# Kernel optimization log

Measured on AMD Instinct MI355X. Metric: run time of the kernel, lower is better.

Reference implementation:

```python
import jax, jax.numpy as jnp
import numpy as np

D = 1024
H = 16
HD = D // H
LN_EPS = 1e-5
RMS_EPS = 1e-6


def layernorm(x, g, b):
    mu = jnp.mean(x, axis=-1, keepdims=True)
    var = jnp.mean(jnp.square(x - mu), axis=-1, keepdims=True)
    return (x - mu) * jax.lax.rsqrt(var + LN_EPS) * g + b


def rmsnorm(x, w):
    ms = jnp.mean(jnp.square(x), axis=-1, keepdims=True)
    return x * jax.lax.rsqrt(ms + RMS_EPS) * w


def setup_inputs() -> dict:
    key = jax.random.key(0)
    ks = jax.random.split(key, 8)
    s = 0.02
    ones = jnp.ones((D,), jnp.float32)
    zeros = jnp.zeros((D,), jnp.float32)
    return {
        "query_tokens": jax.random.normal(ks[0], (4, 512, D), jnp.float32),
        "point_features": jax.random.normal(ks[1], (4, 4096, D), jnp.float32),
        "ln_q_g": ones, "ln_q_b": zeros,
        "ln_kv_g": ones, "ln_kv_b": zeros,
        "Wq": jax.random.normal(ks[2], (D, D), jnp.float32) * s, "bq": zeros,
        "Wk": jax.random.normal(ks[3], (D, D), jnp.float32) * s, "bk": zeros,
        "Wv": jax.random.normal(ks[4], (D, D), jnp.float32) * s, "bv": zeros,
        "rms_q_w": ones, "rms_k_w": ones,
        "Wo": jax.random.normal(ks[5], (D, D), jnp.float32) * s, "bo": zeros,
        "ln_mlp_g": ones, "ln_mlp_b": zeros,
        "W1": jax.random.normal(ks[6], (D, 4 * D), jnp.float32) * s,
        "b1": jnp.zeros((4 * D,), jnp.float32),
        "W2": jax.random.normal(ks[7], (4 * D, D), jnp.float32) * s,
        "b2": zeros,
    }


def reference(query_tokens, point_features, ln_q_g, ln_q_b, ln_kv_g, ln_kv_b,
              Wq, bq, Wk, bk, Wv, bv, rms_q_w, rms_k_w, Wo, bo,
              ln_mlp_g, ln_mlp_b, W1, b1, W2, b2):
    B, K, _ = query_tokens.shape
    N = point_features.shape[1]
    q_in = layernorm(query_tokens, ln_q_g, ln_q_b)
    kv_in = layernorm(point_features, ln_kv_g, ln_kv_b)
    q = rmsnorm(q_in @ Wq + bq, rms_q_w)          # [B,K,D]
    k = rmsnorm(kv_in @ Wk + bk, rms_k_w)         # [B,N,D]
    v = kv_in @ Wv + bv                            # [B,N,D]
    q = q.reshape(B, K, H, HD)
    k = k.reshape(B, N, H, HD)
    v = v.reshape(B, N, H, HD)
    scores = jnp.einsum('bkhd,bnhd->bhkn', q, k) / jnp.sqrt(jnp.float32(HD))
    attn = jax.nn.softmax(scores, axis=-1)
    ctx = jnp.einsum('bhkn,bnhd->bkhd', attn, v).reshape(B, K, D)
    out = ctx @ Wo + bo + query_tokens
    h = layernorm(out, ln_mlp_g, ln_mlp_b)
    mlp = jax.nn.gelu(h @ W1 + b1, approximate=False) @ W2 + b2
    return out + mlp
```

## Files before the change

### kernel.cpp

```cpp
#include <hip/hip_runtime.h>
#include <math.h>

#define DD   1024
#define NHD  16
#define HDIM 64
#define BB   4
#define QN   512
#define KVN  4096
#define FF   4096

typedef __attribute__((ext_vector_type(8))) short bf16x8;
typedef __attribute__((ext_vector_type(4))) float f32x4;

__device__ __forceinline__ float b2f(ushort u){
  union { unsigned u32; float f; } x; x.u32 = ((unsigned)u)<<16; return x.f;
}
__device__ __forceinline__ ushort f2b(float f){
  unsigned u = __float_as_uint(f);
  unsigned r = (u + 0x7FFFu + ((u>>16)&1u)) >> 16;
  return (ushort)r;
}
__device__ __forceinline__ float ldx(const void* p, size_t i, int isbf){
  return isbf ? b2f(((const ushort*)p)[i]) : ((const float*)p)[i];
}
__device__ __forceinline__ int detect_bf(const void* gref){
  return ((const unsigned*)gref)[0] == 0x3F803F80u;
}

#if defined(__has_builtin)
#if __has_builtin(__builtin_amdgcn_global_load_lds)
#define HAS_GLL 1
#endif
#endif
#ifndef HAS_GLL
#define HAS_GLL 0
#endif
__device__ __forceinline__ void stage16(const ushort* g, ushort* lds_base, int lane){
#if HAS_GLL
  __builtin_amdgcn_global_load_lds(g, lds_base, 16, 0, 0);
#else
  *(uint4*)(lds_base + lane*8) = *(const uint4*)g;
#endif
}

__device__ __forceinline__ void wave_barrier(){
  asm volatile("" ::: "memory");
  __builtin_amdgcn_s_barrier();
  asm volatile("" ::: "memory");
}

__global__ __launch_bounds__(256)
void prep_all(const void* __restrict__ Wq, const void* __restrict__ Wk,
              const void* __restrict__ Wv, const void* __restrict__ Wo,
              const void* __restrict__ W1, const void* __restrict__ W2,
              ushort* __restrict__ WqT, ushort* __restrict__ WkvT,
              ushort* __restrict__ WoT,
              ushort* __restrict__ W1T, ushort* __restrict__ W2T,
              const void* __restrict__ qtok, const void* __restrict__ pfeat,
              const void* __restrict__ gq, const void* __restrict__ bq,
              const void* __restrict__ gkv, const void* __restrict__ bkv,
              ushort* __restrict__ q_ln, ushort* __restrict__ kv_ln,
              const void* __restrict__ gref)
{
  const int isbf = detect_bf(gref);
  __shared__ __align__(16) ushort tile[64][72];
  __shared__ float r1[4], r2[4];
  int t = threadIdx.x;

  if (blockIdx.x < 3072){
    int bid = blockIdx.x;
    const void* src; ushort* dst; int R, C, tid;
    if (bid < 1024){
      int s = bid >> 8; tid = bid & 255; R = 1024; C = 1024;
      src = (s==0) ? Wq : (s==1) ? Wk : (s==2) ? Wv : Wo;
      dst = (s==0) ? WqT : (s==1) ? WkvT : (s==2) ? (WkvT + (size_t)1024*1024) : WoT;
    } else if (bid < 2048){ tid = bid - 1024; src = W1; dst = W1T; R = 1024; C = 4096; }
    else                  { tid = bid - 2048; src = W2; dst = W2T; R = 4096; C = 1024; }
    int ntx = C >> 6;
    int tx = tid % ntx, ty = tid / ntx;
    int r0 = ty*64, c0 = tx*64;

    if (isbf){
      #pragma unroll
      for (int i=0;i<2;i++){
        int idx = t + i*256;
        int r = idx>>3, ch = idx&7;
        #pragma unroll
        for (int j=0;j<8;j++)
          tile[r][ch*8+j] = ((const ushort*)src)[(size_t)(r0+r)*C + c0 + ch*8 + j];
      }
    } else {
      #pragma unroll
      for (int i=0;i<2;i++){
        int idx = t + i*256;
        int r = idx>>3, ch = idx&7;
        const float* s4 = (const float*)src + (size_t)(r0+r)*C + c0 + ch*8;
        float4 f0 = *(const float4*)s4;
        float4 f1 = *(const float4*)(s4+4);
        tile[r][ch*8+0]=f2b(f0.x); tile[r][ch*8+1]=f2b(f0.y);
        tile[r][ch*8+2]=f2b(f0.z); tile[r][ch*8+3]=f2b(f0.w);
        tile[r][ch*8+4]=f2b(f1.x); tile[r][ch*8+5]=f2b(f1.y);
        tile[r][ch*8+6]=f2b(f1.z); tile[r][ch*8+7]=f2b(f1.w);
      }
    }
    __syncthreads();
    #pragma unroll
    for (int i=0;i<2;i++){
      int idx = t + i*256;
      int c = idx>>3, ch = idx&7;
      __align__(16) ushort tmp[8];
      #pragma unroll
      for (int j=0;j<8;j++) tmp[j] = tile[ch*8+j][c];
      *(uint4*)(dst + (size_t)(c0+c)*R + r0 + ch*8) = *(uint4*)tmp;
    }
    return;
  }

  int row = blockIdx.x - 3072;
  const void* src; const void* g; const void* bb; ushort* dst; int r;
  if (row < BB*QN){ src = qtok;  g = gq;  bb = bq;  dst = q_ln;  r = row; }
  else            { src = pfeat; g = gkv; bb = bkv; dst = kv_ln; r = row - BB*QN; }
  int c0 = t*4;
  float v[4];
  if (isbf){
    #pragma unroll
    for (int i=0;i<4;i++) v[i] = b2f(((const ushort*)src)[(size_t)r*DD + c0 + i]);
  } else {
    float4 f = *(const float4*)((const float*)src + (size_t)r*DD + c0);
    v[0]=f.x; v[1]=f.y; v[2]=f.z; v[3]=f.w;
  }
  float s1=0.f, s2=0.f;
  #pragma unroll
  for (int i=0;i<4;i++){ s1 += v[i]; s2 += v[i]*v[i]; }
  #pragma unroll
  for (int off=32; off; off>>=1){ s1 += __shfl_xor(s1,off,64); s2 += __shfl_xor(s2,off,64); }
  int wave = t>>6;
  if ((t&63)==0){ r1[wave]=s1; r2[wave]=s2; }
  __syncthreads();
  s1 = r1[0]+r1[1]+r1[2]+r1[3];
  s2 = r2[0]+r2[1]+r2[2]+r2[3];
  float mu  = s1 * (1.0f/DD);
  float var = s2 * (1.0f/DD) - mu*mu;
  float rs  = rsqrtf(var + 1e-5f);
  union { ushort u[4]; uint2 w; } pk;
  #pragma unroll
  for (int i=0;i<4;i++)
    pk.u[i] = f2b((v[i]-mu)*rs*ldx(g,c0+i,isbf) + ldx(bb,c0+i,isbf));
  *(uint2*)(dst + (size_t)r*DD + c0) = pk.w;
}

__global__ __launch_bounds__(256)
void rms_all(ushort* __restrict__ qb, const void* __restrict__ wq,
             ushort* __restrict__ kb, const void* __restrict__ wk,
             const void* __restrict__ gref)
{
  const int isbf = detect_bf(gref);
  int row = blockIdx.x, t = threadIdx.x;
  ushort* x; const void* w; int r;
  if (row < BB*QN){ x = qb; w = wq; r = row; }
  else            { x = kb; w = wk; r = row - BB*QN; }
  int c0 = t*4;
  union { ushort u[4]; uint2 w; } in;
  in.w = *(const uint2*)(x + (size_t)r*DD + c0);
  float v[4];
  #pragma unroll
  for (int i=0;i<4;i++) v[i] = b2f(in.u[i]);
  float s2 = 0.f;
  #pragma unroll
  for (int i=0;i<4;i++) s2 += v[i]*v[i];
  #pragma unroll
  for (int off=32; off; off>>=1) s2 += __shfl_xor(s2,off,64);
  __shared__ float r2[4];
  int wave = t>>6;
  if ((t&63)==0) r2[wave]=s2;
  __syncthreads();
  s2 = r2[0]+r2[1]+r2[2]+r2[3];
  float rs = rsqrtf(s2*(1.0f/DD) + 1e-6f);
  union { ushort u[4]; uint2 w; } pk;
  #pragma unroll
  for (int i=0;i<4;i++) pk.u[i] = f2b(v[i]*rs*ldx(w,c0+i,isbf));
  *(uint2*)(x + (size_t)r*DD + c0) = pk.w;
}

__global__ __launch_bounds__(256)
void ln_combine(const float* __restrict__ parts,
                const void* __restrict__ bo, const void* __restrict__ qtok,
                const void* __restrict__ g, const void* __restrict__ bb,
                float* __restrict__ outb, ushort* __restrict__ y,
                const void* __restrict__ gref)
{
  const int isbf = detect_bf(gref);
  const size_t PSZ = (size_t)BB*QN*DD;
  int row = blockIdx.x, t = threadIdx.x;
  int c0 = t*4;
  size_t base = (size_t)row*DD + c0;
  float v[4] = {0.f,0.f,0.f,0.f};
  #pragma unroll
  for (int z=0; z<4; z++){
    float4 p = *(const float4*)(parts + (size_t)z*PSZ + base);
    v[0]+=p.x; v[1]+=p.y; v[2]+=p.z; v[3]+=p.w;
  }
  if (isbf){
    #pragma unroll
    for (int i=0;i<4;i++)
      v[i] += b2f(((const ushort*)qtok)[base+i]) + b2f(((const ushort*)bo)[c0+i]);
  } else {
    float4 q4 = *(const float4*)((const float*)qtok + base);
    v[0] += q4.x + ((const float*)bo)[c0+0];
    v[1] += q4.y + ((const float*)bo)[c0+1];
    v[2] += q4.z + ((const float*)bo)[c0+2];
    v[3] += q4.w + ((const float*)bo)[c0+3];
  }
  float4 ov; ov.x=v[0]; ov.y=v[1]; ov.z=v[2]; ov.w=v[3];
  *(float4*)(outb + base) = ov;

  float s1=0.f, s2=0.f;
  #pragma unroll
  for (int i=0;i<4;i++){ s1 += v[i]; s2 += v[i]*v[i]; }
  #pragma unroll
  for (int off=32; off; off>>=1){ s1 += __shfl_xor(s1,off,64); s2 += __shfl_xor(s2,off,64); }
  __shared__ float r1[4], r2[4];
  int wave = t>>6;
  if ((t&63)==0){ r1[wave]=s1; r2[wave]=s2; }
  __syncthreads();
  s1 = r1[0]+r1[1]+r1[2]+r1[3];
  s2 = r2[0]+r2[1]+r2[2]+r2[3];
  float mu  = s1 * (1.0f/DD);
  float var = s2 * (1.0f/DD) - mu*mu;
  float rs  = rsqrtf(var + 1e-5f);
  union { ushort u[4]; uint2 w; } pk;
  #pragma unroll
  for (int i=0;i<4;i++)
    pk.u[i] = f2b((v[i]-mu)*rs*ldx(g,c0+i,isbf) + ldx(bb,c0+i,isbf));
  *(uint2*)(y + base) = pk.w;
}

__global__ __launch_bounds__(256)
void combine_w2(const float* __restrict__ P0, const float* __restrict__ P1,
                const float* __restrict__ P2, const void* __restrict__ b2,
                const float* __restrict__ res, void* __restrict__ out,
                const void* __restrict__ gref)
{
  const int isbf = detect_bf(gref);
  const size_t PSZ = (size_t)BB*QN*DD;
  size_t i = ((size_t)blockIdx.x*256 + threadIdx.x)*4;
  float4 v = *(const float4*)(P0 + i);
  #pragma unroll
  for (int z=1; z<4; z++){
    float4 p = *(const float4*)(P0 + (size_t)z*PSZ + i);
    v.x+=p.x; v.y+=p.y; v.z+=p.z; v.w+=p.w;
  }
  #pragma unroll
  for (int z=0; z<2; z++){
    float4 p = *(const float4*)(P1 + (size_t)z*PSZ + i);
    v.x+=p.x; v.y+=p.y; v.z+=p.z; v.w+=p.w;
  }
  #pragma unroll
  for (int z=0; z<2; z++){
    float4 p = *(const float4*)(P2 + (size_t)z*PSZ + i);
    v.x+=p.x; v.y+=p.y; v.z+=p.z; v.w+=p.w;
  }
  float4 r = *(const float4*)(res + i);
  int col = (int)(i & (DD-1));
  v.x += r.x + ldx(b2,col+0,isbf);
  v.y += r.y + ldx(b2,col+1,isbf);
  v.z += r.z + ldx(b2,col+2,isbf);
  v.w += r.w + ldx(b2,col+3,isbf);
  if (isbf){
    union { ushort u[4]; uint2 w; } pk;
    pk.u[0]=f2b(v.x); pk.u[1]=f2b(v.y); pk.u[2]=f2b(v.z); pk.u[3]=f2b(v.w);
    *(uint2*)((ushort*)out + i) = pk.w;
  } else {
    *(float4*)((float*)out + i) = v;
  }
}

template<int ACT_GELU, int OUT_MODE, int RES_MODE>
__global__ __launch_bounds__(256)
void gemm_bt(const ushort* __restrict__ A, const ushort* __restrict__ BT,
             const void* __restrict__ bias,
             const void* __restrict__ res_ext, const float* __restrict__ res_f,
             void* __restrict__ Cout, void* __restrict__ Cout2,
             int M, int N, int Kdim, int Kstride,
             const void* __restrict__ gref)
{
  const int isbf = detect_bf(gref);
  __shared__ __align__(16) ushort As[128*64];
  __shared__ __align__(16) ushort Bs[128*64];
  const int bm = blockIdx.y * 128;
  const int bn = blockIdx.x * 128;
  const int kz = blockIdx.z;
  const int t = threadIdx.x;
  const int wave = t>>6, lane = t&63, quad = lane>>4, l16 = lane&15;
  const int wm = (wave&1)*64, wn = (wave>>1)*64;

  const ushort* ga[4]; const ushort* gb[4];
  #pragma unroll
  for (int j=0;j<4;j++){
    int row = (t>>3) + j*32;
    int g = ((t&7) - row) & 7;
    ga[j] = A  + (size_t)(bm+row)*Kstride + kz*Kdim + g*8;
    gb[j] = BT + (size_t)(bn+row)*Kstride + kz*Kdim + g*8;
  }

  int offA[2][4], offB[2][4];
  #pragma unroll
  for (int kk=0;kk<2;kk++)
    #pragma unroll
    for (int i=0;i<4;i++){
      int ra = wm + i*16 + l16;
      offA[kk][i] = ra*64 + ((quad + kk*4 + ra)&7)*8;
      int rb = wn + i*16 + l16;
      offB[kk][i] = rb*64 + ((quad + kk*4 + rb)&7)*8;
    }

  f32x4 zero = {0.f,0.f,0.f,0.f};
  f32x4 acc[4][4];
  #pragma unroll
  for (int i=0;i<4;i++)
    #pragma unroll
    for (int j=0;j<4;j++) acc[i][j] = zero;

  const int kiters = Kdim >> 6;
  for (int ki = 0; ki < kiters; ki++) {
    #pragma unroll
    for (int j=0;j<4;j++){
      stage16(ga[j], As + (size_t)(j*256 + wave*64)*8, lane);
      stage16(gb[j], Bs + (size_t)(j*256 + wave*64)*8, lane);
      ga[j] += 64; gb[j] += 64;
    }
    __syncthreads();
    #pragma unroll
    for (int kk=0;kk<2;kk++){
      bf16x8 af[4], bfr[4];
      #pragma unroll
      for (int i=0;i<4;i++){
        af[i]  = *(const bf16x8*)(As + offA[kk][i]);
        bfr[i] = *(const bf16x8*)(Bs + offB[kk][i]);
      }
      #pragma unroll
      for (int mt=0;mt<4;mt++)
        #pragma unroll
        for (int nt=0;nt<4;nt++)
          acc[mt][nt] = __builtin_amdgcn_mfma_f32_16x16x32_bf16(af[mt], bfr[nt], acc[mt][nt], 0,0,0);
    }
    __syncthreads();
  }

  if (OUT_MODE == 4){
    float* P = (float*)Cout + (size_t)kz*M*N;
    #pragma unroll
    for (int mt=0;mt<4;mt++){
      #pragma unroll
      for (int r=0;r<4;r++){
        int row = bm + wm + mt*16 + quad*4 + r;
        #pragma unroll
        for (int nt=0;nt<4;nt++){
          int col = bn + wn + nt*16 + l16;
          P[(size_t)row*N + col] = acc[mt][nt][r];
        }
      }
    }
    return;
  }

  float bv[4];
  #pragma unroll
  for (int nt=0;nt<4;nt++) bv[nt] = ldx(bias, bn + wn + nt*16 + l16, isbf);
  #pragma unroll
  for (int mt=0;mt<4;mt++){
    #pragma unroll
    for (int r=0;r<4;r++){
      int row = bm + wm + mt*16 + quad*4 + r;
      #pragma unroll
      for (int nt=0;nt<4;nt++){
        int col = bn + wn + nt*16 + l16;
        float v = acc[mt][nt][r] + bv[nt];
        if (ACT_GELU) v = 0.5f*v*(1.0f + erff(v*0.70710678118f));
        size_t oi = (size_t)row*N + col;
        if (RES_MODE==1) v += ldx(res_ext, oi, isbf);
        if (RES_MODE==2) v += res_f[oi];
        if (OUT_MODE==0)      ((ushort*)Cout)[oi] = f2b(v);
        else if (OUT_MODE==1) ((float*)Cout)[oi]  = v;
        else { if (isbf) ((ushort*)Cout)[oi] = f2b(v); else ((float*)Cout)[oi] = v; }
      }
    }
  }
}

#define G_HB  32768
#define G_RA0 0
#define G_RA1 8192
#define G_RB0 16384
#define G_RB1 24576

#define G_STAGE(src, R, tile) do{ \
  ushort* _d = ldsb + (((tile)&1)*G_HB + (R) + wave*1024); \
  stage16(src[0] + ((tile)<<6), _d,       lane); \
  stage16(src[1] + ((tile)<<6), _d + 512, lane); \
}while(0)

#define G_LDA(dst, base) \
  _Pragma("unroll") for (int kk=0;kk<2;kk++) \
  _Pragma("unroll") for (int m=0;m<4;m++) \
    dst[kk][m] = *(const bf16x8*)((base) + offA[kk][m]);

#define G_LDB(dst, base) \
  _Pragma("unroll") for (int kk=0;kk<2;kk++) \
  _Pragma("unroll") for (int n=0;n<2;n++) \
    dst[kk][n] = *(const bf16x8*)((base) + offB[kk][n]);

#define G_MM16(ar, br, MO, NO) \
  _Pragma("unroll") for (int kk=0;kk<2;kk++) \
  _Pragma("unroll") for (int m=0;m<4;m++) \
  _Pragma("unroll") for (int n=0;n<2;n++) \
    acc[m+(MO)][n+(NO)] = __builtin_amdgcn_mfma_f32_16x16x32_bf16(ar[kk][m], br[kk][n], acc[m+(MO)][n+(NO)], 0,0,0);

#define G_SYNC() do{ wave_barrier(); \
  __builtin_amdgcn_s_setprio(1); }while(0)

#define G_END() do{ __builtin_amdgcn_s_setprio(0); wave_barrier(); }while(0)

template<int MODE>
__global__ __launch_bounds__(512, 2)
void gemm256(const ushort* __restrict__ A, const ushort* __restrict__ BT,
             const void* __restrict__ biasK, const void* __restrict__ biasV,
             ushort* __restrict__ Kout, ushort* __restrict__ Vt,
             float* __restrict__ P0, float* __restrict__ P1,
             float* __restrict__ P2,
             int Kdim, int Kstride,
             const void* __restrict__ gref)
{
  const int isbf = detect_bf(gref);
  __shared__ __align__(16) ushort ldsb[65536];
  const int nb = blockIdx.x;
  int bx, by, kz = 0;
  if (MODE == 0){
    int k = nb & 7, j = nb >> 3;
    int kvid = 64*k + j; bx = kvid & 7; by = kvid >> 3;
  } else {
    int wsw = (nb & 7)*32 + (nb >> 3);
    bx = wsw & 3; by = (wsw >> 2) & 7; kz = wsw >> 5;
  }
  const int bmrow = by*256;
  const int bn = bx*256;
  const int koff = (MODE==1) ? kz*Kdim : 0;
  const int t = threadIdx.x;
  const int wave = t>>6, lane = t&63, quad = lane>>4, l16 = lane&15;
  const int wg = wave>>2, wn = wave&3;

  const ushort *sA0[2], *sA1[2], *sB0[2], *sB1[2];
  #pragma unroll
  for (int jj=0;jj<2;jj++){
    int r = (wave*2 + jj)*8 + (lane>>3);
    int g = ((lane&7) - r) & 7;
    int grA0 = r + (r & 64);
    int gc0  = (r & 31) + ((r >> 5) << 6);
    sA0[jj] = A  + (size_t)(bmrow + grA0     )*Kstride + koff + g*8;
    sA1[jj] = A  + (size_t)(bmrow + grA0 + 64)*Kstride + koff + g*8;
    sB0[jj] = BT + (size_t)(bn + gc0      )*Kstride + koff + g*8;
    sB1[jj] = BT + (size_t)(bn + gc0 + 32 )*Kstride + koff + g*8;
  }

  int offA[2][4], offB[2][2];
  #pragma unroll
  for (int kk=0;kk<2;kk++){
    int slot = ((kk*4 + quad + l16) & 7) * 8;
    #pragma unroll
    for (int m=0;m<4;m++) offA[kk][m] = (wg*64 + m*16 + l16)*64 + slot;
    #pragma unroll
    for (int n=0;n<2;n++) offB[kk][n] = (wn*32 + n*16 + l16)*64 + slot;
  }

  f32x4 zero = {0.f,0.f,0.f,0.f};
  f32x4 acc[8][4];
  #pragma unroll
  for (int i=0;i<8;i++)
    #pragma unroll
    for (int j=0;j<4;j++) acc[i][j] = zero;

  G_STAGE(sA0, G_RA0, 0);
  G_STAGE(sB0, G_RB0, 0);
  G_STAGE(sB1, G_RB1, 0);
  G_STAGE(sA1, G_RA1, 0);
  G_STAGE(sA0, G_RA0, 1);
  G_STAGE(sB1, G_RB1, 1);
  G_STAGE(sA1, G_RA1, 1);
  asm volatile("s_waitcnt vmcnt(6)" ::: "memory");
  wave_barrier();

  const int niter = Kdim >> 7;
  const ushort* L0 = ldsb;
  const ushort* L1 = ldsb + G_HB;
  bf16x8 a[2][4], b[2][2], b1[2][2];

  for (int i = 0; i < niter; ++i) {
    const bool st = (i + 1 < niter);
    G_LDA(a, L0 + G_RA0); G_LDB(b, L0 + G_RB0);
    G_STAGE(sB0, G_RB0, 2*i+1);
    G_SYNC(); G_MM16(a, b, 0, 0); G_END();
    G_LDB(b1, L0 + G_RB1);
    if (st) G_STAGE(sA0, G_RA0, 2*i+2);
    G_SYNC(); G_MM16(a, b1, 0, 2); G_END();
    G_LDA(a, L0 + G_RA1);
    if (st) G_STAGE(sB1, G_RB1, 2*i+2);
    G_SYNC(); G_MM16(a, b1, 4, 2); G_END();
    if (st) G_STAGE(sA1, G_RA1, 2*i+2);
    G_SYNC(); G_MM16(a, b, 4, 0);
    __builtin_amdgcn_s_setprio(0);
    if (st) { asm volatile("s_waitcnt vmcnt(6)" ::: "memory"); }
    else    { asm volatile("s_waitcnt vmcnt(0)" ::: "memory"); }
    wave_barrier();
    G_LDA(a, L1 + G_RA0); G_LDB(b, L1 + G_RB0);
    if (st) G_STAGE(sB0, G_RB0, 2*i+2);
    G_SYNC(); G_MM16(a, b, 0, 0); G_END();
    G_LDB(b1, L1 + G_RB1);
    if (st) G_STAGE(sA0, G_RA0, 2*i+3);
    G_SYNC(); G_MM16(a, b1, 0, 2); G_END();
    G_LDA(a, L1 + G_RA1);
    if (st) G_STAGE(sB1, G_RB1, 2*i+3);
    G_SYNC(); G_MM16(a, b1, 4, 2); G_END();
    if (st) G_STAGE(sA1, G_RA1, 2*i+3);
    G_SYNC(); G_MM16(a, b, 4, 0);
    __builtin_amdgcn_s_setprio(0);
    if (st) { asm volatile("s_waitcnt vmcnt(6)" ::: "memory"); }
    wave_barrier();
  }

  if (MODE == 1){
    const size_t PSZ = (size_t)BB*QN*DD;
    float* P = (kz < 4) ? P0 + (size_t)kz*PSZ
             : (kz < 6) ? P1 + (size_t)(kz-4)*PSZ
                        : P2 + (size_t)(kz-6)*PSZ;
    #pragma unroll
    for (int mt=0;mt<8;mt++){
      #pragma unroll
      for (int r=0;r<4;r++){
        int row = bmrow + wg*128 + mt*16 + quad*4 + r;
        #pragma unroll
        for (int nt=0;nt<4;nt++){
          int col = bn + wn*64 + nt*16 + l16;
          P[(size_t)row*1024 + col] = acc[mt][nt][r];
        }
      }
    }
    return;
  }
  if (bn < 1024){
    float bvv[4];
    #pragma unroll
    for (int nt=0;nt<4;nt++) bvv[nt] = ldx(biasK, bn + wn*64 + nt*16 + l16, isbf);
    #pragma unroll
    for (int mt=0;mt<8;mt++){
      #pragma unroll
      for (int r=0;r<4;r++){
        int row = bmrow + wg*128 + mt*16 + quad*4 + r;
        #pragma unroll
        for (int nt=0;nt<4;nt++){
          int col = bn + wn*64 + nt*16 + l16;
          Kout[(size_t)row*1024 + col] = f2b(acc[mt][nt][r] + bvv[nt]);
        }
      }
    }
  } else {
    float bvv[4];
    #pragma unroll
    for (int nt=0;nt<4;nt++) bvv[nt] = ldx(biasV, bn - 1024 + wn*64 + nt*16 + l16, isbf);
    #pragma unroll
    for (int mt=0;mt<8;mt++){
      int row0 = bmrow + wg*128 + mt*16 + quad*4;
      int bi = row0 >> 12, tok = row0 & (KVN-1);
      #pragma unroll
      for (int nt=0;nt<4;nt++){
        int cl = bn - 1024 + wn*64 + nt*16 + l16;
        union { ushort u[4]; uint2 w2; } pk;
        #pragma unroll
        for (int r=0;r<4;r++) pk.u[r] = f2b(acc[mt][nt][r] + bvv[nt]);
        size_t o = ((size_t)((bi*NHD + (cl>>6))*HDIM + (cl&63)))*KVN + tok;
        *(uint2*)(Vt + o) = pk.w2;
      }
    }
  }
}

__global__ __launch_bounds__(256, 3)
void flash_attn3(const ushort* __restrict__ Q, const ushort* __restrict__ K,
                 const ushort* __restrict__ Vt, float* __restrict__ Op,
                 float* __restrict__ ML)
{
  __shared__ __align__(16) ushort Ks[128*72];
  __shared__ __align__(16) ushort Vs[64*136];
  __shared__ __align__(16) ushort Ps[4][16*136];
  const int bh = blockIdx.x, qt = blockIdx.y, hf = blockIdx.z;
  const int b = bh>>4, h = bh&15;
  const int t = threadIdx.x, wave = t>>6, lane = t&63, quad = lane>>4, l16 = lane&15;
  ushort* Pz = Ps[wave];

  const float QS = 0.125f * 1.4426950408889634f;
  bf16x8 qf[2][2];
  #pragma unroll
  for (int mt=0;mt<2;mt++){
    const ushort* qb = Q + (size_t)(b*QN + qt*128 + wave*32 + mt*16 + l16)*DD + h*HDIM;
    bf16x8 r0 = *(const bf16x8*)(qb + quad*8);
    bf16x8 r1 = *(const bf16x8*)(qb + 32 + quad*8);
    #pragma unroll
    for (int j=0;j<8;j++){
      qf[mt][0][j] = (short)f2b(b2f((ushort)r0[j]) * QS);
      qf[mt][1][j] = (short)f2b(b2f((ushort)r1[j]) * QS);
    }
  }

  f32x4 zero = {0.f,0.f,0.f,0.f};
  f32x4 o[2][4];
  #pragma unroll
  for (int mt=0;mt<2;mt++)
    #pragma unroll
    for (int nt=0;nt<4;nt++) o[mt][nt] = zero;
  float lp[2][4] = {{0.f,0.f,0.f,0.f},{0.f,0.f,0.f,0.f}};

  const ushort* kgb = K  + (size_t)(b*KVN + hf*2048)*DD + h*HDIM;
  const ushort* vtb = Vt + ((size_t)bh*HDIM)*KVN + hf*2048;
  const int kcs = t&7;

  for (int kv0 = 0; kv0 < 2048; kv0 += 128) {
    #pragma unroll
    for (int j=0;j<4;j++){
      int kr = (t>>3) + j*32;
      *(uint4*)(Ks + kr*72 + kcs*8) =
        *(const uint4*)(kgb + (size_t)(kv0+kr)*DD + kcs*8);
    }
    #pragma unroll
    for (int j=0;j<4;j++){
      int p = t + j*256; int vr = p>>4, vc = p&15;
      uint4 d = *(const uint4*)(vtb + (size_t)vr*KVN + kv0 + vc*8);
      ushort* pv = (ushort*)&d;
      ushort* vbp = Vs + vr*136 + (vc&1)*64 + (vc>>1);
      #pragma unroll
      for (int jj=0;jj<8;jj++) vbp[jj*8] = pv[jj];
    }
    __syncthreads();

    f32x4 pb[2][8];
    #pragma unroll
    for (int nt=0;nt<8;nt++){
      const ushort* kb = Ks + (nt*16+l16)*72 + quad*8;
      bf16x8 kf0 = *(const bf16x8*)kb;
      bf16x8 kf1 = *(const bf16x8*)(kb + 32);
      #pragma unroll
      for (int mt=0;mt<2;mt++){
        __builtin_amdgcn_s_setprio(1);
        f32x4 a = __builtin_amdgcn_mfma_f32_16x16x32_bf16(qf[mt][0], kf0, zero, 0,0,0);
        a = __builtin_amdgcn_mfma_f32_16x16x32_bf16(qf[mt][1], kf1, a, 0,0,0);
        __builtin_amdgcn_s_setprio(0);
        #pragma unroll
        for (int r=0;r<4;r++) a[r] = __builtin_amdgcn_exp2f(fminf(a[r], 88.f));
        pb[mt][nt] = a;
      }
    }
    #pragma unroll
    for (int mt=0;mt<2;mt++){
      #pragma unroll
      for (int r=0;r<4;r++){
        float ls = 0.f;
        bf16x8 pk;
        #pragma unroll
        for (int nt=0;nt<8;nt++){
          ls += pb[mt][nt][r];
          pk[nt] = (short)(__float_as_uint(pb[mt][nt][r]) >> 16);
        }
        lp[mt][r] += ls;
        *(bf16x8*)(Pz + (quad*4+r)*136 + l16*8) = pk;
      }
      #pragma unroll
      for (int kc=0;kc<4;kc++){
        bf16x8 pa = *(const bf16x8*)(Pz + l16*136 + kc*32 + quad*8);
        pb[mt][kc] = *(f32x4*)&pa;
      }
    }
    #pragma unroll
    for (int nt=0;nt<4;nt++){
      const ushort* vbr = Vs + (nt*16+l16)*136;
      #pragma unroll
      for (int kc=0;kc<4;kc++){
        bf16x8 vf = *(const bf16x8*)(vbr + kc*32 + quad*8);
        __builtin_amdgcn_s_setprio(1);
        o[0][nt] = __builtin_amdgcn_mfma_f32_16x16x32_bf16(*(bf16x8*)&pb[0][kc], vf, o[0][nt], 0,0,0);
        o[1][nt] = __builtin_amdgcn_mfma_f32_16x16x32_bf16(*(bf16x8*)&pb[1][kc], vf, o[1][nt], 0,0,0);
        __builtin_amdgcn_s_setprio(0);
      }
    }
    __syncthreads();
  }

  const int slot = hf*256 + bh*4 + qt;
  float* Ob = Op + (size_t)slot*128*64;
  #pragma unroll
  for (int mt=0;mt<2;mt++)
    #pragma unroll
    for (int nt=0;nt<4;nt++)
      #pragma unroll
      for (int r=0;r<4;r++)
        Ob[(wave*32 + mt*16 + quad*4 + r)*64 + nt*16 + l16] = o[mt][nt][r];
  #pragma unroll
  for (int mt=0;mt<2;mt++)
    #pragma unroll
    for (int r=0;r<4;r++){
      float v = lp[mt][r];
      #pragma unroll
      for (int off=1; off<16; off<<=1) v += __shfl_xor(v, off, 64);
      if (l16 == 0)
        ML[(size_t)slot*128 + wave*32 + mt*16 + quad*4 + r] = v;
    }
}

__global__ __launch_bounds__(256)
void flash_combine4(const float* __restrict__ Op, const float* __restrict__ ML,
                    ushort* __restrict__ Ctx)
{
  const int bq = blockIdx.x;
  const int bh = bq>>2, qt = bq&3;
  const int b = bh>>4, h = bh&15;
  const int t = threadIdx.x;
  const int row = t>>1, hd0 = (t&1)*32;
  float l = 0.f;
  #pragma unroll
  for (int i=0;i<2;i++) l += ML[(size_t)(i*256 + bq)*128 + row];
  float inv = 1.0f / l;
  float4 a[8];
  #pragma unroll
  for (int c=0;c<8;c++){ a[c].x=0.f; a[c].y=0.f; a[c].z=0.f; a[c].w=0.f; }
  #pragma unroll
  for (int i=0;i<2;i++){
    const float* s = Op + ((size_t)(i*256 + bq)*128 + row)*64 + hd0;
    #pragma unroll
    for (int c=0;c<8;c++){
      float4 v = *(const float4*)(s + c*4);
      a[c].x += v.x; a[c].y += v.y; a[c].z += v.z; a[c].w += v.w;
    }
  }
  ushort* dst = Ctx + (size_t)(b*QN + qt*128 + row)*DD + h*HDIM + hd0;
  #pragma unroll
  for (int c=0;c<8;c++){
    union { ushort u[4]; uint2 w; } pk;
    pk.u[0] = f2b(a[c].x*inv); pk.u[1] = f2b(a[c].y*inv);
    pk.u[2] = f2b(a[c].z*inv); pk.u[3] = f2b(a[c].w*inv);
    *(uint2*)(dst + c*4) = pk.w;
  }
}

extern "C" void kernel_launch(void* const* d_in, const int* in_sizes, int n_in,
                              void* d_out, int out_size, void* d_ws, size_t ws_size,
                              hipStream_t stream)
{
  const void* qtok    = d_in[0];
  const void* pfeat   = d_in[1];
  const void* ln_q_g  = d_in[2];
  const void* ln_q_b  = d_in[3];
  const void* ln_kv_g = d_in[4];
  const void* ln_kv_b = d_in[5];
  const void* Wq      = d_in[6];
  const void* bq      = d_in[7];
  const void* Wk      = d_in[8];
  const void* bk      = d_in[9];
  const void* Wv      = d_in[10];
  const void* bv      = d_in[11];
  const void* rms_q_w = d_in[12];
  const void* rms_k_w = d_in[13];
  const void* Wo      = d_in[14];
  const void* bo      = d_in[15];
  const void* ln_mlp_g= d_in[16];
  const void* ln_mlp_b= d_in[17];
  const void* W1      = d_in[18];
  const void* b1      = d_in[19];
  const void* W2      = d_in[20];
  const void* b2      = d_in[21];
  const void* gref    = ln_q_g;

  char* w = (char*)d_ws;
  auto take = [&](size_t bytes)->char*{ char* p = w; w += (bytes + 255) & ~(size_t)255; return p; };
  ushort* WqT  = (ushort*)take((size_t)DD*DD*2);
  ushort* WkvT = (ushort*)take((size_t)2*DD*DD*2);
  ushort* WoT  = (ushort*)take((size_t)DD*DD*2);
  ushort* W1T  = (ushort*)take((size_t)DD*FF*2);
  ushort* W2T  = (ushort*)take((size_t)FF*DD*2);
  ushort* kv_ln= (ushort*)take((size_t)BB*KVN*DD*2);
  ushort* q_ln = (ushort*)take((size_t)BB*QN*DD*2);
  ushort* kbuf = (ushort*)take((size_t)BB*KVN*DD*2);
  ushort* qbuf = (ushort*)take((size_t)BB*QN*DD*2);
  ushort* Vt   = (ushort*)take((size_t)BB*KVN*DD*2);
  ushort* ctx  = WqT;
  float*  outb = (float*)kbuf;
  ushort* mlp1 = kv_ln;
  float*  Op   = (float*)kv_ln;
  float*  ML   = (float*)q_ln;
  float*  o_parts  = (float*)kv_ln;
  ushort* h_ln = q_ln;
  float*  w2p0 = (float*)Vt;
  float*  w2p1 = (float*)(kv_ln + (size_t)8*1024*1024);
  float*  w2p2 = (float*)d_ws;

  prep_all<<<3072 + BB*QN + BB*KVN,256,0,stream>>>(
      Wq,Wk,Wv,Wo,W1,W2, WqT,WkvT,WoT,W1T,W2T,
      qtok,pfeat, ln_q_g,ln_q_b, ln_kv_g,ln_kv_b, q_ln, kv_ln, gref);
  gemm_bt<0,0,0><<<dim3(8,16), 256,0,stream>>>(q_ln,  WqT, bq, nullptr,nullptr,
                                               qbuf, nullptr, BB*QN, DD, DD, DD, gref);
  gemm256<0><<<512, 512, 0, stream>>>(kv_ln, WkvT, bk, bv, kbuf, Vt,
                                      nullptr, nullptr, nullptr, DD, DD, gref);
  rms_all<<<BB*QN + BB*KVN,256,0,stream>>>(qbuf, rms_q_w, kbuf, rms_k_w, gref);
  flash_attn3<<<dim3(64,4,2),256,0,stream>>>(qbuf, kbuf, Vt, Op, ML);
  flash_combine4<<<256,256,0,stream>>>(Op, ML, ctx);
  gemm_bt<0,4,0><<<dim3(8,16,4),256,0,stream>>>(ctx, WoT, nullptr, nullptr,nullptr,
                                                o_parts, nullptr, BB*QN, DD, DD/4, DD, gref);
  ln_combine<<<BB*QN,256,0,stream>>>(o_parts, bo, qtok, ln_mlp_g, ln_mlp_b,
                                     outb, h_ln, gref);
  gemm_bt<1,0,0><<<dim3(32,16),256,0,stream>>>(h_ln, W1T, b1, nullptr,nullptr,
                                               mlp1, nullptr, BB*QN, FF, DD, DD, gref);
  gemm256<1><<<256, 512, 0, stream>>>(mlp1, W2T, nullptr, nullptr,
                                      nullptr, nullptr,
                                      w2p0, w2p1, w2p2, FF/8, FF, gref);
  combine_w2<<<BB*QN*DD/1024,256,0,stream>>>(w2p0, w2p1, w2p2, b2, outb, d_out, gref);
}
```

Measured before the change: 486.3 us.

## Prefetch next K/V tile into registers during attention compute

Restructures the attention KV loop so the next 128-row K and V tiles are loaded from global memory into registers while the current tile is used for the MFMA work. The registers are written to shared memory after the trailing barrier. This is meant to hide global load latency behind the matrix math. The cost is 8 extra uint4 registers per thread, which raises register pressure and may reduce occupancy.

```diff
diff --git a/kernel.cpp b/kernel.cpp
--- a/kernel.cpp
+++ b/kernel.cpp
@@ -622,23 +622,42 @@
   const ushort* vtb = Vt + ((size_t)bh*HDIM)*KVN + hf*2048;
   const int kcs = t&7;
 
-  for (int kv0 = 0; kv0 < 2048; kv0 += 128) {
-    #pragma unroll
-    for (int j=0;j<4;j++){
-      int kr = (t>>3) + j*32;
-      *(uint4*)(Ks + kr*72 + kcs*8) =
-        *(const uint4*)(kgb + (size_t)(kv0+kr)*DD + kcs*8);
-    }
-    #pragma unroll
-    for (int j=0;j<4;j++){
-      int p = t + j*256; int vr = p>>4, vc = p&15;
-      uint4 d = *(const uint4*)(vtb + (size_t)vr*KVN + kv0 + vc*8);
-      ushort* pv = (ushort*)&d;
-      ushort* vbp = Vs + vr*136 + (vc&1)*64 + (vc>>1);
-      #pragma unroll
-      for (int jj=0;jj<8;jj++) vbp[jj*8] = pv[jj];
-    }
+  int krr[4], vrr[4], vcc[4];
+  #pragma unroll
+  for (int j=0;j<4;j++){
+    krr[j] = (t>>3) + j*32;
+    int p = t + j*256; vrr[j] = p>>4; vcc[j] = p&15;
+  }
+
+  uint4 kpre[4], vpre[4];
+  #pragma unroll
+  for (int j=0;j<4;j++)
+    kpre[j] = *(const uint4*)(kgb + (size_t)krr[j]*DD + kcs*8);
+  #pragma unroll
+  for (int j=0;j<4;j++)
+    vpre[j] = *(const uint4*)(vtb + (size_t)vrr[j]*KVN + vcc[j]*8);
+  #pragma unroll
+  for (int j=0;j<4;j++)
+    *(uint4*)(Ks + krr[j]*72 + kcs*8) = kpre[j];
+  #pragma unroll
+  for (int j=0;j<4;j++){
+    ushort* pv = (ushort*)&vpre[j];
+    ushort* vbp = Vs + vrr[j]*136 + (vcc[j]&1)*64 + (vcc[j]>>1);
+    #pragma unroll
+    for (int jj=0;jj<8;jj++) vbp[jj*8] = pv[jj];
+  }
+
+  for (int it = 0; it < 16; ++it) {
     __syncthreads();
+    if (it + 1 < 16){
+      int nv = (it+1)*128;
+      #pragma unroll
+      for (int j=0;j<4;j++)
+        kpre[j] = *(const uint4*)(kgb + (size_t)(nv+krr[j])*DD + kcs*8);
+      #pragma unroll
+      for (int j=0;j<4;j++)
+        vpre[j] = *(const uint4*)(vtb + (size_t)vrr[j]*KVN + nv + vcc[j]*8);
+    }
 
     f32x4 pb[2][8];
     #pragma unroll
@@ -690,6 +709,18 @@
       }
     }
     __syncthreads();
+    if (it + 1 < 16){
+      #pragma unroll
+      for (int j=0;j<4;j++)
+        *(uint4*)(Ks + krr[j]*72 + kcs*8) = kpre[j];
+      #pragma unroll
+      for (int j=0;j<4;j++){
+        ushort* pv = (ushort*)&vpre[j];
+        ushort* vbp = Vs + vrr[j]*136 + (vcc[j]&1)*64 + (vcc[j]>>1);
+        #pragma unroll
+        for (int jj=0;jj<8;jj++) vbp[jj*8] = pv[jj];
+      }
+    }
   }
 
   const int slot = hf*256 + bh*4 + qt;
```

Measured after the change: 499.3 us. 2.7% more time.
